# Optimization experiments

Measured on AMD Instinct MI355X. Metric: run time of the kernel, lower is better.

## Reference

```python
import jax, jax.numpy as jnp
import numpy as np
from functools import partial
from jax import lax

THRESHOLD = 1.0
BETA = 4.0

@partial(jax.custom_vjp, nondiff_argnums=(1, 2))
def spike_fn(membrane, threshold, beta):
    # hard threshold forward
    return (membrane >= threshold).astype(membrane.dtype)

def _spike_fwd(membrane, threshold, beta):
    return spike_fn(membrane, threshold, beta), membrane

def _spike_bwd(threshold, beta, membrane, g):
    # fast-sigmoid surrogate gradient: 1 / (1 + beta*|u - theta|)^2
    x = membrane - threshold
    surrogate = 1.0 / (1.0 + beta * jnp.abs(x)) ** 2
    return (g * surrogate,)

spike_fn.defvjp(_spike_fwd, _spike_bwd)


def setup_inputs() -> dict:
    key = jax.random.key(0)
    k1, = jax.random.split(key, 1)
    x = jax.random.normal(k1, (64, 100, 4096), dtype=jnp.float32)
    # log_alpha = log(exp(-1/tau_mem)) = -1/tau_mem, tau_mem = 20.0
    log_alpha = jnp.asarray(-1.0 / 20.0, dtype=jnp.float32)
    return {"x": x, "log_alpha": log_alpha}


def reference(x, log_alpha):
    # x: (batch, time, features)
    alpha = jax.nn.sigmoid(log_alpha)  # membrane decay in (0,1)

    def step(u, xt):
        u = alpha * u + xt                    # leaky integration
        s = spike_fn(u, THRESHOLD, BETA)      # fire
        u = u - s * THRESHOLD                 # subtract-reset
        return u, s

    x_t = jnp.swapaxes(x, 0, 1)               # (T, B, F)
    u0 = jnp.zeros_like(x_t[0])
    _, spikes_t = lax.scan(step, u0, x_t)
    spikes = jnp.swapaxes(spikes_t, 0, 1)      # (B, T, F)
    rate = spikes.mean()
    return spikes, rate
```

## Files before the change

kernel.cpp:

```cpp
#include <hip/hip_runtime.h>
#include <math.h>


constexpr int T_STEPS = 100;
constexpr int CHUNK   = 20;
constexpr int NCHUNK  = T_STEPS / CHUNK;
constexpr int F       = 4096;
constexpr int BATCH   = 64;
constexpr int NBLOCKS = BATCH * F / 256;
constexpr long long TOTAL = (long long)BATCH * T_STEPS * F;

__global__ __launch_bounds__(256)
void lif_fwd(const float* __restrict__ x,
             const float* __restrict__ log_alpha,
             float*       __restrict__ out,
             unsigned int* __restrict__ blk_cnt) {
    int idx  = blockIdx.x * 256 + threadIdx.x;
    int b    = idx >> 12;
    int f    = idx & 4095;
    size_t base = (size_t)b * T_STEPS * F + f;

    double la = (double)log_alpha[0];
    float alpha = (float)(1.0 / (1.0 + exp(-la)));

    float u = 0.f;
    unsigned int mask[4] = {0u, 0u, 0u, 0u};

    float bufA[CHUNK], bufB[CHUNK];

    #pragma unroll
    for (int j = 0; j < CHUNK; ++j)
        bufA[j] = x[base + (size_t)j * F];

    #pragma unroll
    for (int c = 0; c < NCHUNK; ++c) {
        float* cur = (c & 1) ? bufB : bufA;
        float* nxt = (c & 1) ? bufA : bufB;
        if (c + 1 < NCHUNK) {
            #pragma unroll
            for (int j = 0; j < CHUNK; ++j)
                nxt[j] = x[base + (size_t)((c + 1) * CHUNK + j) * F];
        }
        #pragma unroll
        for (int j = 0; j < CHUNK; ++j) {
            int t = c * CHUNK + j;
            u = __fadd_rn(__fmul_rn(alpha, u), cur[j]);
            unsigned int bit = (u >= 1.0f) ? 1u : 0u;
            mask[t >> 5] |= bit << (t & 31);
            u -= (u >= 1.0f) ? 1.0f : 0.0f;
        }
    }

    #pragma unroll
    for (int t = 0; t < T_STEPS; ++t) {
        float s = ((mask[t >> 5] >> (t & 31)) & 1u) ? 1.0f : 0.0f;
        out[base + (size_t)t * F] = s;
    }

    unsigned int c = (unsigned)__popc(mask[0]) + (unsigned)__popc(mask[1])
                   + (unsigned)__popc(mask[2]) + (unsigned)__popc(mask[3]);

    for (int off = 32; off > 0; off >>= 1)
        c += __shfl_down(c, off, 64);

    __shared__ unsigned int wsum[4];
    int lane = threadIdx.x & 63;
    int wid  = threadIdx.x >> 6;
    if (lane == 0) wsum[wid] = c;
    __syncthreads();
    if (threadIdx.x == 0)
        blk_cnt[blockIdx.x] = wsum[0] + wsum[1] + wsum[2] + wsum[3];
}

__global__ __launch_bounds__(256)
void lif_rate(const unsigned int* __restrict__ blk_cnt,
              float* __restrict__ rate_out) {
    unsigned int c = 0;
    #pragma unroll
    for (int i = 0; i < NBLOCKS / 256; ++i)
        c += blk_cnt[threadIdx.x + i * 256];
    for (int off = 32; off > 0; off >>= 1)
        c += __shfl_down(c, off, 64);
    __shared__ unsigned int wsum[4];
    int lane = threadIdx.x & 63;
    int wid  = threadIdx.x >> 6;
    if (lane == 0) wsum[wid] = c;
    __syncthreads();
    if (threadIdx.x == 0) {
        unsigned int s = wsum[0] + wsum[1] + wsum[2] + wsum[3];
        rate_out[0] = (float)((double)s / (double)TOTAL);
    }
}

extern "C" void kernel_launch(void* const* d_in, const int* in_sizes, int n_in,
                              void* d_out, int out_size, void* d_ws, size_t ws_size,
                              hipStream_t stream) {
    const float* x  = (const float*)d_in[0];
    const float* la = (const float*)d_in[1];
    float* out = (float*)d_out;
    unsigned int* blk_cnt = (unsigned int*)d_ws;

    lif_fwd<<<NBLOCKS, 256, 0, stream>>>(x, la, out, blk_cnt);
    lif_rate<<<1, 256, 0, stream>>>(blk_cnt, out + TOTAL);
}
```

Baseline: 39.04 us.

## Transpose spike masks across lanes for vectorized nontemporal float4 output stores

Result: faster. 38.11 us (-2.4%).

```diff
diff --git a/kernel.cpp b/kernel.cpp
--- a/kernel.cpp
+++ b/kernel.cpp
@@ -1,6 +1,8 @@
 #include <hip/hip_runtime.h>
 #include <math.h>
 
+
+typedef float f32x4 __attribute__((ext_vector_type(4)));
 
 constexpr int T_STEPS = 100;
 constexpr int CHUNK   = 20;
@@ -51,21 +53,52 @@
         }
     }
 
-    #pragma unroll
-    for (int t = 0; t < T_STEPS; ++t) {
-        float s = ((mask[t >> 5] >> (t & 31)) & 1u) ? 1.0f : 0.0f;
-        out[base + (size_t)t * F] = s;
-    }
-
     unsigned int c = (unsigned)__popc(mask[0]) + (unsigned)__popc(mask[1])
                    + (unsigned)__popc(mask[2]) + (unsigned)__popc(mask[3]);
+
+    int lane = threadIdx.x & 63;
+    int q = lane >> 4;
+    int r = lane & 15;
+
+    unsigned int m0[4], m1[4], m2[4], m3[4];
+    #pragma unroll
+    for (int j = 0; j < 4; ++j) {
+        m0[j] = __shfl(mask[0], 4 * r + j, 64);
+        m1[j] = __shfl(mask[1], 4 * r + j, 64);
+        m2[j] = __shfl(mask[2], 4 * r + j, 64);
+        m3[j] = __shfl(mask[3], 4 * r + j, 64);
+    }
+    unsigned int lo[4], hi[4];
+    #pragma unroll
+    for (int j = 0; j < 4; ++j) {
+        lo[j] = (q <= 1) ? m0[j] : (q == 2 ? m1[j] : m2[j]);
+        hi[j] = (q == 0) ? m0[j] : (q == 1 ? m1[j] : (q == 2 ? m2[j] : m3[j]));
+    }
+    int lo_idx = (25 * q) >> 5;
+
+    int fwave = (blockIdx.x * 256 + (threadIdx.x & ~63)) & 4095;
+    size_t sbase = (size_t)b * T_STEPS * F + fwave + 4 * r;
+
+    #pragma unroll
+    for (int i = 0; i < 25; ++i) {
+        int t  = 25 * q + i;
+        bool use_lo = ((t >> 5) == lo_idx);
+        int tb = t & 31;
+        f32x4 s;
+        #pragma unroll
+        for (int j = 0; j < 4; ++j) {
+            unsigned int w = use_lo ? lo[j] : hi[j];
+            s[j] = (float)((w >> tb) & 1u);
+        }
+        __builtin_nontemporal_store(
+            s, reinterpret_cast<f32x4*>(&out[sbase + (size_t)t * F]));
+    }
 
     for (int off = 32; off > 0; off >>= 1)
         c += __shfl_down(c, off, 64);
 
     __shared__ unsigned int wsum[4];
-    int lane = threadIdx.x & 63;
-    int wid  = threadIdx.x >> 6;
+    int wid = threadIdx.x >> 6;
     if (lane == 0) wsum[wid] = c;
     __syncthreads();
     if (threadIdx.x == 0)
```
